# Optimization experiments

Measured on AMD Instinct MI355X. Metric: run time of the kernel, lower is better.

The kernel has to match this reference:

```python
import jax, jax.numpy as jnp
from jax import lax
import numpy as np

WS = (4, 4, 4)          # window size (wd, wh, ww)
DIM = 192               # input channels
HEADS = 6
EPS = 1e-5


def _rel_pos_index(ws):
    coords = np.stack(np.meshgrid(np.arange(ws[0]), np.arange(ws[1]), np.arange(ws[2]), indexing='ij'))
    flat = coords.reshape(3, -1)                              # (3, N)
    rel = (flat[:, :, None] - flat[:, None, :]).transpose(1, 2, 0).astype(np.int64)  # (N, N, 3)
    rel[..., 0] += ws[0] - 1
    rel[..., 1] += ws[1] - 1
    rel[..., 2] += ws[2] - 1
    rel[..., 0] *= (2 * ws[1] - 1) * (2 * ws[2] - 1)
    rel[..., 1] *= (2 * ws[2] - 1)
    return jnp.asarray(rel.sum(-1))                           # (N, N)

REL_IDX = _rel_pos_index(WS)


def _ln(x, g, b):
    m = x.mean(-1, keepdims=True)
    v = x.var(-1, keepdims=True)
    return (x - m) * lax.rsqrt(v + EPS) * g + b


def _inorm(x):  # InstanceNorm3d, affine=False: normalize over spatial dims per (b, c)
    m = x.mean(axis=(2, 3, 4), keepdims=True)
    v = x.var(axis=(2, 3, 4), keepdims=True)
    return (x - m) * lax.rsqrt(v + EPS)


def _gelu(x):
    return jax.nn.gelu(x, approximate=False)


def _win_to_vol(xw, b, d, h, w):
    # (b*d*h*w, wd*wh*ww, c) -> (b, c, d*wd, h*wh, w*ww)
    wd, wh, ww = WS
    c = xw.shape[-1]
    x = xw.reshape(b, d, h, w, wd, wh, ww, c)
    x = x.transpose(0, 7, 1, 4, 2, 5, 3, 6)
    return x.reshape(b, c, d * wd, h * wh, w * ww)


def _vol_to_win(vol):
    # (b, c, D, H, W) -> (b*d*h*w, wd*wh*ww, c)
    wd, wh, ww = WS
    b, c, Dv, Hv, Wv = vol.shape
    x = vol.reshape(b, c, Dv // wd, wd, Hv // wh, wh, Wv // ww, ww)
    x = x.transpose(0, 2, 4, 6, 3, 5, 7, 1)
    return x.reshape(-1, wd * wh * ww, c)


def _conv1x1(x, w, b):  # x: (b,c,D,H,W), w: (c_in, c_out)
    return jnp.einsum('bcdhw,co->bodhw', x, w) + b[None, :, None, None, None]


def _forward(x, w_pattn, b_pattn, g_aln, b_aln, w_pcnn, b_pcnn, g_cln, b_cln,
             dw_w, dw_b, ci_w1, ci_b1, ci_w2, ci_b2, pj_w, pj_b, qkv_w, qkv_b,
             si_w1, si_b1, si_w2, si_b2, g_anorm, b_anorm, w_proj, b_proj, rpb,
             D, H, W):
    wd, wh, ww = WS
    d, h, w = D // wd, H // wh, W // ww
    Bwin, N, _ = x.shape
    b = Bwin // (d * h * w)

    x_atten = _ln(x @ w_pattn + b_pattn, g_aln, b_aln)          # (Bwin, N, 96)
    x_cnn = _ln(x @ w_pcnn + b_pcnn, g_cln, b_cln)              # (Bwin, N, 192)

    vol = _win_to_vol(x_cnn, b, d, h, w)                        # (b, 192, D, H, W)
    vol = lax.conv_general_dilated(vol, dw_w, (1, 1, 1), [(1, 1)] * 3,
                                   feature_group_count=DIM,
                                   dimension_numbers=('NCDHW', 'OIDHW', 'NCDHW'))
    vol = vol + dw_b[None, :, None, None, None]
    vol = _gelu(_inorm(vol))

    pooled = vol.mean(axis=(2, 3, 4))                           # (b, 192)
    ci = _gelu(pooled @ ci_w1 + ci_b1) @ ci_w2 + ci_b2          # (b, 96)
    x_cnn = _conv1x1(vol, pj_w, pj_b)                           # (b, 96, D, H, W)

    C = x_atten.shape[-1]
    hd = C // HEADS
    qkv = (x_atten @ qkv_w + qkv_b).reshape(Bwin, N, 3, HEADS, hd).transpose(2, 0, 3, 1, 4)
    q, k, v = qkv[0], qkv[1], qkv[2]                            # (Bwin, heads, N, hd)

    gate = jax.nn.sigmoid(ci).reshape(b, 1, HEADS, 1, hd)
    v = (v.reshape(b, -1, HEADS, N, hd) * gate).reshape(Bwin, HEADS, N, hd)

    attn = jnp.einsum('bhnd,bhmd->bhnm', q * (hd ** -0.5), k)
    bias = rpb[REL_IDX.reshape(-1)].reshape(N, N, HEADS).transpose(2, 0, 1)
    attn = jax.nn.softmax(attn + bias[None], axis=-1)
    x_atten = jnp.einsum('bhnm,bhmd->bnhd', attn, v).reshape(Bwin, N, C)

    sp = _win_to_vol(x_atten, b, d, h, w)                       # (b, 96, D, H, W)
    si = _conv1x1(sp, si_w1, si_b1)
    si = _gelu(_inorm(si))
    si = _conv1x1(si, si_w2, si_b2)                             # (b, 1, D, H, W)
    x_cnn = _inorm(jax.nn.sigmoid(si) * x_cnn)
    x_cnn = _vol_to_win(x_cnn)                                  # (Bwin, N, 96)

    x_atten = _ln(x_atten, g_anorm, b_anorm)
    return jnp.concatenate([x_atten, x_cnn], axis=-1) @ w_proj + b_proj


def setup_inputs() -> dict:
    key = jax.random.key(0)
    ks = jax.random.split(key, 16)
    def p(i, shape, s=0.02):
        return jax.random.normal(ks[i], shape, jnp.float32) * s
    return {
        'x': jax.random.normal(ks[0], (2048, 64, 192), jnp.float32),
        'w_pattn': p(1, (192, 96)), 'b_pattn': jnp.zeros((96,), jnp.float32),
        'g_aln': jnp.ones((96,), jnp.float32), 'b_aln': jnp.zeros((96,), jnp.float32),
        'w_pcnn': p(2, (192, 192)), 'b_pcnn': jnp.zeros((192,), jnp.float32),
        'g_cln': jnp.ones((192,), jnp.float32), 'b_cln': jnp.zeros((192,), jnp.float32),
        'dw_w': p(3, (192, 1, 3, 3, 3)), 'dw_b': jnp.zeros((192,), jnp.float32),
        'ci_w1': p(4, (192, 24)), 'ci_b1': jnp.zeros((24,), jnp.float32),
        'ci_w2': p(5, (24, 96)), 'ci_b2': jnp.zeros((96,), jnp.float32),
        'pj_w': p(6, (192, 96)), 'pj_b': jnp.zeros((96,), jnp.float32),
        'qkv_w': p(7, (96, 288)), 'qkv_b': jnp.zeros((288,), jnp.float32),
        'si_w1': p(8, (96, 12)), 'si_b1': jnp.zeros((12,), jnp.float32),
        'si_w2': p(9, (12, 1)), 'si_b2': jnp.zeros((1,), jnp.float32),
        'g_anorm': jnp.ones((96,), jnp.float32), 'b_anorm': jnp.zeros((96,), jnp.float32),
        'w_proj': p(10, (192, 192)), 'b_proj': jnp.zeros((192,), jnp.float32),
        'rpb': p(11, (343, 6)),
        'D': 32, 'H': 32, 'W': 32,
    }


def reference(x, w_pattn, b_pattn, g_aln, b_aln, w_pcnn, b_pcnn, g_cln, b_cln,
              dw_w, dw_b, ci_w1, ci_b1, ci_w2, ci_b2, pj_w, pj_b, qkv_w, qkv_b,
              si_w1, si_b1, si_w2, si_b2, g_anorm, b_anorm, w_proj, b_proj, rpb,
              D, H, W):
    return _forward(x, w_pattn, b_pattn, g_aln, b_aln, w_pcnn, b_pcnn, g_cln, b_cln,
                    dw_w, dw_b, ci_w1, ci_b1, ci_w2, ci_b2, pj_w, pj_b, qkv_w, qkv_b,
                    si_w1, si_b1, si_w2, si_b2, g_anorm, b_anorm, w_proj, b_proj, rpb,
                    D, H, W)
```

## Files before the change

kernel.cpp:

```cpp
#include <hip/hip_runtime.h>
#include <hip/hip_bf16.h>
#include <math.h>

#define EPS 1e-5f
#define XAS 97
#define QS 17
#define SS 65

typedef __attribute__((ext_vector_type(8))) short short8;
typedef __attribute__((ext_vector_type(4))) float f32x4;

__device__ __forceinline__ float gelu_f(float x){
    return 0.5f*x*(1.0f+erff(x*0.7071067811865475f));
}
__device__ __forceinline__ float sigmoid_f(float x){
    return 1.0f/(1.0f+__expf(-x));
}
__device__ __forceinline__ int row_to_bv(int r){
    int wi = r >> 6, n = r & 63;
    int b = wi >> 9, rem = wi & 511;
    int zd = rem >> 6, yh = (rem >> 3) & 7, xw = rem & 7;
    int wz = n >> 4, wy = (n >> 2) & 3, wx = n & 3;
    int Dz = (zd<<2)+wz, Hy = (yh<<2)+wy, Wx = (xw<<2)+wx;
    return (b<<15) + (Dz<<10) + (Hy<<5) + Wx;
}
__device__ __forceinline__ int relidx(int i,int j){
    int zi=i>>4, yi=(i>>2)&3, xi=i&3;
    int zj=j>>4, yj=(j>>2)&3, xj=j&3;
    return ((zi-zj+3)*7+(yi-yj+3))*7+(xi-xj+3);
}
__device__ __forceinline__ void split8(const float* p, short8& hi, short8& lo){
    union{short8 v; __hip_bfloat16 b[8];} uh, ul;
    #pragma unroll
    for(int i=0;i<8;i++){
        float v=p[i];
        __hip_bfloat16 h=__float2bfloat16(v);
        uh.b[i]=h;
        ul.b[i]=__float2bfloat16(v-__bfloat162float(h));
    }
    hi=uh.v; lo=ul.v;
}

__global__ __launch_bounds__(256) void kprep1(const float* __restrict__ w1,
    const float* __restrict__ w2, __hip_bfloat16* __restrict__ WThi,
    __hip_bfloat16* __restrict__ WTlo)
{
    int i=blockIdx.x*256+threadIdx.x;
    int n=i/192, k=i-n*192;
    float v=(n<96)? w1[k*96+n] : w2[k*192+(n-96)];
    __hip_bfloat16 hb=__float2bfloat16(v);
    WThi[i]=hb;
    WTlo[i]=__float2bfloat16(v-__bfloat162float(hb));
}

__global__ __launch_bounds__(256) void kprepq(const float* __restrict__ w,
    __hip_bfloat16* __restrict__ WThi, __hip_bfloat16* __restrict__ WTlo)
{
    int i=blockIdx.x*256+threadIdx.x;
    int n=i/96, k=i-n*96;
    float v=w[k*288+n];
    __hip_bfloat16 hb=__float2bfloat16(v);
    WThi[i]=hb;
    WTlo[i]=__float2bfloat16(v-__bfloat162float(hb));
}

__global__ __launch_bounds__(256) void kprepp(const float* __restrict__ w,
    __hip_bfloat16* __restrict__ WThi, __hip_bfloat16* __restrict__ WTlo)
{
    int i=blockIdx.x*256+threadIdx.x;
    int n=i/192, k=i-n*192;
    float v=w[k*96+n];
    __hip_bfloat16 hb=__float2bfloat16(v);
    WThi[i]=hb;
    WTlo[i]=__float2bfloat16(v-__bfloat162float(hb));
}


__global__ __launch_bounds__(256,4) void k1_mfma(const float* __restrict__ x,
    const __hip_bfloat16* __restrict__ WThi, const __hip_bfloat16* __restrict__ WTlo,
    const float* __restrict__ b1, const float* __restrict__ g1, const float* __restrict__ bb1,
    const float* __restrict__ b2, const float* __restrict__ g2, const float* __restrict__ bb2,
    float* __restrict__ xa, float* __restrict__ vol)
{
    __shared__ short bs[288*64];
    int tid=threadIdx.x;
    int row0=blockIdx.x*64;
    int wave=tid>>6, lane=tid&63, quad=lane>>4, l16=lane&15;
    const short* Whi=(const short*)WThi;
    const short* Wlo=(const short*)WTlo;
    f32x4 acc[18];
    #pragma unroll
    for(int j=0;j<18;j++) acc[j]=(f32x4){0.f,0.f,0.f,0.f};
    const float* aptr = x + (size_t)(row0+wave*16+l16)*192 + quad*8;
    int rbase = l16*64 + ((quad ^ (l16&7))<<3);
    for(int t=0;t<6;t++){
        float av[8];
        *(f32x4*)&av[0]=*(const f32x4*)(aptr + t*32);
        *(f32x4*)&av[4]=*(const f32x4*)(aptr + t*32 + 4);
        if(t) __syncthreads();
        #pragma unroll
        for(int it=0;it<9;it++){
            int u=tid+it*256;
            int n=u>>3, gi=u&7;
            const short* src=(gi<4?Whi:Wlo) + n*192 + t*32 + (gi&3)*8;
            *(short8*)&bs[n*64 + ((gi^(n&7))<<3)] = *(const short8*)src;
        }
        __syncthreads();
        short8 ahi, alo;
        split8(av, ahi, alo);
        #pragma unroll
        for(int j=0;j<18;j++){
            int idx=j*1024+rbase;
            short8 bhi = *(const short8*)&bs[idx];
            short8 blo = *(const short8*)&bs[idx^32];
            acc[j]=__builtin_amdgcn_mfma_f32_16x16x32_bf16(ahi,bhi,acc[j],0,0,0);
            acc[j]=__builtin_amdgcn_mfma_f32_16x16x32_bf16(ahi,blo,acc[j],0,0,0);
            acc[j]=__builtin_amdgcn_mfma_f32_16x16x32_bf16(alo,bhi,acc[j],0,0,0);
        }
    }
    float bias[18];
    #pragma unroll
    for(int j=0;j<18;j++){ int c=j*16+l16; bias[j]=(c<96)? b1[c] : b2[c-96]; }
    #pragma unroll
    for(int reg=0; reg<4; reg++){
        int grow=row0 + wave*16 + quad*4 + reg;
        float va[6];
        float s=0.f, ss=0.f;
        #pragma unroll
        for(int j=0;j<6;j++){ float v=acc[j][reg]+bias[j]; va[j]=v; s+=v; ss+=v*v; }
        #pragma unroll
        for(int o=1;o<16;o<<=1){ s+=__shfl_xor(s,o); ss+=__shfl_xor(ss,o); }
        float m=s*(1.f/96.f), var=ss*(1.f/96.f)-m*m, rstd=rsqrtf(var+EPS);
        #pragma unroll
        for(int j=0;j<6;j++){
            int c=j*16+l16;
            xa[(size_t)grow*96+c]=(va[j]-m)*rstd*g1[c]+bb1[c];
        }
        float vc[12];
        s=0.f; ss=0.f;
        #pragma unroll
        for(int j=0;j<12;j++){ float v=acc[6+j][reg]+bias[6+j]; vc[j]=v; s+=v; ss+=v*v; }
        #pragma unroll
        for(int o=1;o<16;o<<=1){ s+=__shfl_xor(s,o); ss+=__shfl_xor(ss,o); }
        float m2=s*(1.f/192.f), var2=ss*(1.f/192.f)-m2*m2, rstd2=rsqrtf(var2+EPS);
        int bv=row_to_bv(grow);
        #pragma unroll
        for(int j=0;j<12;j++){
            int c=j*16+l16;
            vol[(size_t)bv*192+c]=(vc[j]-m2)*rstd2*g2[c]+bb2[c];
        }
    }
}

__global__ __launch_bounds__(192) void k2_dwconv(const float* __restrict__ vin,
        const float* __restrict__ wd_, const float* __restrict__ bd,
        float* __restrict__ vout)
{
    int c=threadIdx.x;
    int blk=blockIdx.x;
    int Hy=blk&31, Dz=(blk>>5)&31, b=blk>>10;
    float wreg[27];
    #pragma unroll
    for(int t=0;t<27;t++) wreg[t]=wd_[c*27+t];
    float bias=bd[c];
    const float* base=vin + ((size_t)b<<15)*192;
    int voff[9]; bool vld[9];
    #pragma unroll
    for(int i=0;i<9;i++){
        int zz=Dz+i/3-1, yy=Hy+i%3-1;
        vld[i]=(zz>=0&&zz<32&&yy>=0&&yy<32);
        voff[i]=(zz<<10)+(yy<<5);
    }
    float prv[9],cur[9],nxt[9];
    #pragma unroll
    for(int i=0;i<9;i++){
        prv[i]=0.f;
        cur[i]= vld[i]? base[(size_t)(voff[i])*192+c]   : 0.f;
        nxt[i]= vld[i]? base[(size_t)(voff[i]+1)*192+c] : 0.f;
    }
    size_t obase=((size_t)((b<<15)+(Dz<<10)+(Hy<<5)))*192 + c;
    for(int wx=0;wx<32;wx++){
        float o=bias;
        #pragma unroll
        for(int i=0;i<9;i++) o += prv[i]*wreg[i*3] + cur[i]*wreg[i*3+1] + nxt[i]*wreg[i*3+2];
        vout[obase + (size_t)wx*192] = o;
        #pragma unroll
        for(int i=0;i<9;i++){ prv[i]=cur[i]; cur[i]=nxt[i]; }
        int wn=wx+2;
        #pragma unroll
        for(int i=0;i<9;i++) nxt[i]=(vld[i]&&wn<32)? base[(size_t)(voff[i]+wn)*192+c] : 0.f;
    }
}

__global__ __launch_bounds__(192) void k3_stats(const float* __restrict__ v,
      float* __restrict__ sum, float* __restrict__ sumsq)
{
    int c=threadIdx.x;
    int chunk=blockIdx.x, b=blockIdx.y;
    float s=0.f,ss=0.f;
    const float* p = v + (((size_t)b<<15) + (size_t)chunk*256)*192 + c;
    for(int i=0;i<256;i++){ float t=p[(size_t)i*192]; s+=t; ss+=t*t; }
    atomicAdd(&sum[b*192+c], s);
    atomicAdd(&sumsq[b*192+c], ss);
}

__global__ void k_finalize(const float* __restrict__ sum, const float* __restrict__ sumsq,
                           float* __restrict__ mean, float* __restrict__ rstd, int n, float inv)
{
    int i = blockIdx.x*blockDim.x + threadIdx.x;
    if(i<n){ float m=sum[i]*inv; float v=sumsq[i]*inv - m*m; mean[i]=m; rstd[i]=rsqrtf(v+EPS); }
}

__global__ __launch_bounds__(192) void k4_apply(float* __restrict__ v,
      const float* __restrict__ mean, const float* __restrict__ rstd, float* __restrict__ pooled)
{
    int c=threadIdx.x; int chunk=blockIdx.x, b=blockIdx.y;
    float m=mean[b*192+c], r=rstd[b*192+c];
    float s=0.f;
    float* p = v + (((size_t)b<<15)+(size_t)chunk*256)*192 + c;
    for(int i=0;i<256;i++){
        float t=(p[(size_t)i*192]-m)*r;
        t=gelu_f(t);
        p[(size_t)i*192]=t; s+=t;
    }
    atomicAdd(&pooled[b*192+c], s);
}

__global__ __launch_bounds__(128) void k4b_gate(const float* __restrict__ pooled,
   const float* __restrict__ w1,const float* __restrict__ b1,
   const float* __restrict__ w2,const float* __restrict__ b2, float* __restrict__ gate)
{
    __shared__ float pm[192];
    __shared__ float h[24];
    int b=blockIdx.x, t=threadIdx.x;
    for(int i=t;i<192;i+=128) pm[i]=pooled[b*192+i]*(1.f/32768.f);
    __syncthreads();
    if(t<24){ float a=b1[t]; for(int k=0;k<192;k++) a+=pm[k]*w1[k*24+t]; h[t]=gelu_f(a); }
    __syncthreads();
    if(t<96){ float a=b2[t]; for(int j=0;j<24;j++) a+=h[j]*w2[j*96+t]; gate[b*96+t]=sigmoid_f(a); }
}

__global__ __launch_bounds__(256,4) void kqkv(const float* __restrict__ xa,
    const __hip_bfloat16* __restrict__ WThi, const __hip_bfloat16* __restrict__ WTlo,
    const float* __restrict__ bias_, const float* __restrict__ gate,
    __hip_bfloat16* __restrict__ qkv)
{
    __shared__ short bs[288*64];
    int tid=threadIdx.x;
    int row0=blockIdx.x*64;
    int wave=tid>>6, lane=tid&63, quad=lane>>4, l16=lane&15;
    const short* Whi=(const short*)WThi;
    const short* Wlo=(const short*)WTlo;
    f32x4 acc[18];
    #pragma unroll
    for(int j=0;j<18;j++) acc[j]=(f32x4){0.f,0.f,0.f,0.f};
    const float* aptr = xa + (size_t)(row0+wave*16+l16)*96 + quad*8;
    int rbase = l16*64 + ((quad ^ (l16&7))<<3);
    for(int t=0;t<3;t++){
        float av[8];
        *(f32x4*)&av[0]=*(const f32x4*)(aptr + t*32);
        *(f32x4*)&av[4]=*(const f32x4*)(aptr + t*32 + 4);
        if(t) __syncthreads();
        #pragma unroll
        for(int it=0;it<9;it++){
            int u=tid+it*256;
            int n=u>>3, gi=u&7;
            const short* src=(gi<4?Whi:Wlo) + n*96 + t*32 + (gi&3)*8;
            *(short8*)&bs[n*64 + ((gi^(n&7))<<3)] = *(const short8*)src;
        }
        __syncthreads();
        short8 ahi, alo;
        split8(av, ahi, alo);
        #pragma unroll
        for(int j=0;j<18;j++){
            int idx=j*1024+rbase;
            short8 bhi = *(const short8*)&bs[idx];
            short8 blo = *(const short8*)&bs[idx^32];
            acc[j]=__builtin_amdgcn_mfma_f32_16x16x32_bf16(ahi,bhi,acc[j],0,0,0);
            acc[j]=__builtin_amdgcn_mfma_f32_16x16x32_bf16(ahi,blo,acc[j],0,0,0);
            acc[j]=__builtin_amdgcn_mfma_f32_16x16x32_bf16(alo,bhi,acc[j],0,0,0);
        }
    }
    int b = row0>>15;
    float gv[6];
    #pragma unroll
    for(int j=0;j<6;j++) gv[j]=gate[b*96 + j*16 + l16];
    #pragma unroll
    for(int j=0;j<18;j++){
        float bb=bias_[j*16+l16];
        int which=j/6;
        #pragma unroll
        for(int reg=0;reg<4;reg++){
            int row=row0+wave*16+quad*4+reg;
            int wi=row>>6, n=row&63;
            float v=acc[j][reg]+bb;
            if(which==0) v*=0.25f;
            else if(which==2) v*=gv[j-12];
            qkv[((size_t)(wi*18+j)<<10) + (n<<4) + l16]=__float2bfloat16(v);
        }
    }
}

__global__ __launch_bounds__(256) void k6_attn(const __hip_bfloat16* __restrict__ qkv,
    const float* __restrict__ rpb, float* __restrict__ ato)
{
    __shared__ float sq[64*QS], sk[64*QS], sv[64*QS];
    __shared__ float sS[64*SS];
    int tid=threadIdx.x;
    int wi=blockIdx.x;
    for(int h=0;h<6;h++){
        __syncthreads();
        for(int i=tid;i<3*1024;i+=256){
            int which=i>>10, r=i&1023; int n=r>>4, e=r&15;
            float val=__bfloat162float(qkv[((size_t)(wi*18+which*6+h)<<10) + r]);
            if(which==0) sq[n*QS+e]=val; else if(which==1) sk[n*QS+e]=val; else sv[n*QS+e]=val;
        }
        __syncthreads();
        {
            int ti=tid>>4, tj=tid&15;
            int i0=ti*4, j0=tj*4;
            float a[4][4]={};
            #pragma unroll
            for(int e=0;e<16;e++){
                float qv[4], kv[4];
                #pragma unroll
                for(int ii=0;ii<4;ii++) qv[ii]=sq[(i0+ii)*QS+e];
                #pragma unroll
                for(int jj=0;jj<4;jj++) kv[jj]=sk[(j0+jj)*QS+e];
                #pragma unroll
                for(int ii=0;ii<4;ii++)
                    #pragma unroll
                    for(int jj=0;jj<4;jj++) a[ii][jj]+=qv[ii]*kv[jj];
            }
            #pragma unroll
            for(int ii=0;ii<4;ii++)
                #pragma unroll
                for(int jj=0;jj<4;jj++)
                    sS[(i0+ii)*SS+j0+jj]=a[ii][jj]+rpb[relidx(i0+ii,j0+jj)*6+h];
        }
        __syncthreads();
        {
            int i=tid>>2, j0=(tid&3)<<4;
            float mx=-1e30f;
            for(int jj=0;jj<16;jj++) mx=fmaxf(mx,sS[i*SS+j0+jj]);
            for(int o=1;o<4;o<<=1) mx=fmaxf(mx,__shfl_xor(mx,o));
            float sum=0.f;
            for(int jj=0;jj<16;jj++){float p=__expf(sS[i*SS+j0+jj]-mx); sS[i*SS+j0+jj]=p; sum+=p;}
            for(int o=1;o<4;o<<=1) sum+=__shfl_xor(sum,o);
            float inv=1.f/sum;
            for(int jj=0;jj<16;jj++) sS[i*SS+j0+jj]*=inv;
        }
        __syncthreads();
        {
            int i=tid&63, e0=(tid>>6)<<2;
            float o0=0.f,o1=0.f,o2=0.f,o3=0.f;
            for(int j=0;j<64;j++){
                float p=sS[i*SS+j];
                o0+=p*sv[j*QS+e0];o1+=p*sv[j*QS+e0+1];o2+=p*sv[j*QS+e0+2];o3+=p*sv[j*QS+e0+3];
            }
            float* dst=&ato[((size_t)(wi*64+i))*96 + (h<<4) + e0];
            dst[0]=o0;dst[1]=o1;dst[2]=o2;dst[3]=o3;
        }
    }
}

__global__ __launch_bounds__(256) void k5_pj(const float* __restrict__ vin,
    const __hip_bfloat16* __restrict__ WThi, const __hip_bfloat16* __restrict__ WTlo,
    const float* __restrict__ bias_, float* __restrict__ out)
{
    __shared__ short bs[96*64];
    int tid=threadIdx.x;
    int row0=blockIdx.x*64;
    int wave=tid>>6, lane=tid&63, quad=lane>>4, l16=lane&15;
    const short* Whi=(const short*)WThi;
    const short* Wlo=(const short*)WTlo;
    f32x4 acc[6];
    #pragma unroll
    for(int j=0;j<6;j++) acc[j]=(f32x4){0.f,0.f,0.f,0.f};
    const float* aptr = vin + (size_t)(row0+wave*16+l16)*192 + quad*8;
    int rbase = l16*64 + ((quad ^ (l16&7))<<3);
    for(int t=0;t<6;t++){
        float av[8];
        *(f32x4*)&av[0]=*(const f32x4*)(aptr + t*32);
        *(f32x4*)&av[4]=*(const f32x4*)(aptr + t*32 + 4);
        if(t) __syncthreads();
        #pragma unroll
        for(int it=0;it<3;it++){
            int u=tid+it*256;
            int n=u>>3, gi=u&7;
            const short* src=(gi<4?Whi:Wlo) + n*192 + t*32 + (gi&3)*8;
            *(short8*)&bs[n*64 + ((gi^(n&7))<<3)] = *(const short8*)src;
        }
        __syncthreads();
        short8 ahi, alo;
        split8(av, ahi, alo);
        #pragma unroll
        for(int j=0;j<6;j++){
            int idx=j*1024+rbase;
            short8 bhi = *(const short8*)&bs[idx];
            short8 blo = *(const short8*)&bs[idx^32];
            acc[j]=__builtin_amdgcn_mfma_f32_16x16x32_bf16(ahi,bhi,acc[j],0,0,0);
            acc[j]=__builtin_amdgcn_mfma_f32_16x16x32_bf16(ahi,blo,acc[j],0,0,0);
            acc[j]=__builtin_amdgcn_mfma_f32_16x16x32_bf16(alo,bhi,acc[j],0,0,0);
        }
    }
    #pragma unroll
    for(int j=0;j<6;j++){
        int cc=j*16+l16;
        float bb=bias_[cc];
        #pragma unroll
        for(int reg=0;reg<4;reg++){
            int row=row0+wave*16+quad*4+reg;
            out[(size_t)row*96+cc]=acc[j][reg]+bb;
        }
    }
}

__global__ __launch_bounds__(192) void k7a_si(const float* __restrict__ ato,
    const float* __restrict__ w1, const float* __restrict__ b1,
    float* __restrict__ si12, float* __restrict__ siSum, float* __restrict__ siSumsq)
{
    __shared__ float sa[64*XAS];
    __shared__ float sw[96*12];
    __shared__ float red[24];
    int tid=threadIdx.x, wi=blockIdx.x, b=wi>>9;
    for(int i=tid;i<64*96;i+=192){ int n=i/96,c=i-n*96; sa[n*XAS+c]=ato[((size_t)(wi*64+n))*96+c]; }
    for(int i=tid;i<96*12;i+=192) sw[i]=w1[i];
    if(tid<24) red[tid]=0.f;
    __syncthreads();
    #pragma unroll
    for(int j=0;j<4;j++){
        int o=tid+192*j; int n=o/12, cc=o-n*12;
        float a=b1[cc];
        for(int k=0;k<96;k++) a+=sa[n*XAS+k]*sw[k*12+cc];
        atomicAdd(&red[cc],a);
        atomicAdd(&red[12+cc],a*a);
        int bv=row_to_bv(wi*64+n);
        si12[(size_t)bv*12+cc]=a;
    }
    __syncthreads();
    if(tid<12){ atomicAdd(&siSum[b*12+tid],red[tid]); atomicAdd(&siSumsq[b*12+tid],red[12+tid]); }
}

__global__ __launch_bounds__(256) void k7d_sig(const float* __restrict__ si12,
  const float* __restrict__ mean, const float* __restrict__ rstd,
  const float* __restrict__ w2, const float* __restrict__ b2, float* __restrict__ sig)
{
    int bv=blockIdx.x*256+threadIdx.x;
    int b=bv>>15;
    float a=b2[0];
    #pragma unroll
    for(int c=0;c<12;c++){
        float t=(si12[(size_t)bv*12+c]-mean[b*12+c])*rstd[b*12+c];
        a+=gelu_f(t)*w2[c];
    }
    sig[bv]=sigmoid_f(a);
}

__global__ __launch_bounds__(192) void k8_gstats(const float* __restrict__ pj,
   const float* __restrict__ sig, float* __restrict__ gSum, float* __restrict__ gSumsq)
{
    int tid=threadIdx.x; int c=tid%96, vh=tid/96;
    int chunk=blockIdx.x, b=blockIdx.y;
    float s=0.f,ss=0.f;
    for(int i=0;i<128;i++){
        int v=chunk*256 + i*2 + vh;
        int bv=(b<<15)+v;
        float t=sig[bv]*pj[(size_t)bv*96+c];
        s+=t; ss+=t*t;
    }
    atomicAdd(&gSum[b*96+c],s); atomicAdd(&gSumsq[b*96+c],ss);
}

__global__ __launch_bounds__(256) void kprep(const float* __restrict__ wp,
                                             __hip_bfloat16* __restrict__ WT)
{
    int i=blockIdx.x*256+threadIdx.x;
    int n=i/192, k=i-n*192;
    WT[n*192+k]=__float2bfloat16(wp[k*192+n]);
}

__global__ __launch_bounds__(256) void k9a2_gather(float* atoU,
  const float* __restrict__ pj, const float* __restrict__ sig,
  const float* __restrict__ gMean, const float* __restrict__ gRstd,
  const float* __restrict__ ga, const float* __restrict__ bba)
{
    int tid=threadIdx.x; int row0=blockIdx.x*32;
    int rr=tid>>3, part=tid&7;
    int r=row0+rr;
    __hip_bfloat16* U=(__hip_bfloat16*)atoU;
    float av[12];
    #pragma unroll
    for(int j=0;j<12;j++) av[j]=atoU[(size_t)r*96+part*12+j];
    float s=0.f, ss=0.f;
    #pragma unroll
    for(int j=0;j<12;j++){ s+=av[j]; ss+=av[j]*av[j]; }
    #pragma unroll
    for(int o=1;o<8;o<<=1){ s+=__shfl_xor(s,o); ss+=__shfl_xor(ss,o); }
    float m=s*(1.f/96.f), var=ss*(1.f/96.f)-m*m, rstd=rsqrtf(var+EPS);
    int bv=row_to_bv(r); int b=bv>>15;
    float sg=sig[bv];
    float cv[12];
    #pragma unroll
    for(int j=0;j<12;j++){
        int c=part*12+j;
        float t=sg*pj[(size_t)bv*96+c];
        cv[j]=(t-gMean[b*96+c])*gRstd[b*96+c];
    }
    #pragma unroll
    for(int j=0;j<12;j++){
        int c=part*12+j;
        U[(size_t)r*192+c]=__float2bfloat16((av[j]-m)*rstd*ga[c]+bba[c]);
    }
    #pragma unroll
    for(int j=0;j<12;j++){
        int c=part*12+j;
        U[(size_t)r*192+96+c]=__float2bfloat16(cv[j]);
    }
}

__global__ __launch_bounds__(256) void k9b_mfma(const __hip_bfloat16* __restrict__ Ubf,
   const __hip_bfloat16* __restrict__ WT, const float* __restrict__ bp,
   float* __restrict__ out)
{
    int tid=threadIdx.x;
    int wave=tid>>6, lane=tid&63;
    int quad=lane>>4, l16=lane&15;
    int rowA = blockIdx.x*64 + wave*16 + l16;
    const short* Us=(const short*)Ubf;
    const short* Ws=(const short*)WT;
    f32x4 acc[12];
    #pragma unroll
    for(int j=0;j<12;j++) acc[j]=(f32x4){0.f,0.f,0.f,0.f};
    #pragma unroll
    for(int t=0;t<6;t++){
        int k0=t*32;
        short8 a = *(const short8*)(Us + (size_t)rowA*192 + k0 + quad*8);
        #pragma unroll
        for(int j=0;j<12;j++){
            short8 bfr = *(const short8*)(Ws + (size_t)(j*16+l16)*192 + k0 + quad*8);
            acc[j]=__builtin_amdgcn_mfma_f32_16x16x32_bf16(a,bfr,acc[j],0,0,0);
        }
    }
    int mbase = blockIdx.x*64 + wave*16 + quad*4;
    #pragma unroll
    for(int j=0;j<12;j++){
        int n=j*16+l16;
        float bias=bp[n];
        #pragma unroll
        for(int r2=0;r2<4;r2++){
            out[(size_t)(mbase+r2)*192 + n] = acc[j][r2] + bias;
        }
    }
}

extern "C" void kernel_launch(void* const* d_in, const int* in_sizes, int n_in,
                              void* d_out, int out_size, void* d_ws, size_t ws_size,
                              hipStream_t stream)
{
    const float* x      =(const float*)d_in[0];
    const float* w_pattn=(const float*)d_in[1];
    const float* b_pattn=(const float*)d_in[2];
    const float* g_aln  =(const float*)d_in[3];
    const float* b_aln  =(const float*)d_in[4];
    const float* w_pcnn =(const float*)d_in[5];
    const float* b_pcnn =(const float*)d_in[6];
    const float* g_cln  =(const float*)d_in[7];
    const float* b_cln  =(const float*)d_in[8];
    const float* dw_w   =(const float*)d_in[9];
    const float* dw_b   =(const float*)d_in[10];
    const float* ci_w1  =(const float*)d_in[11];
    const float* ci_b1  =(const float*)d_in[12];
    const float* ci_w2  =(const float*)d_in[13];
    const float* ci_b2  =(const float*)d_in[14];
    const float* pj_w   =(const float*)d_in[15];
    const float* pj_b   =(const float*)d_in[16];
    const float* qkv_w  =(const float*)d_in[17];
    const float* qkv_b  =(const float*)d_in[18];
    const float* si_w1  =(const float*)d_in[19];
    const float* si_b1  =(const float*)d_in[20];
    const float* si_w2  =(const float*)d_in[21];
    const float* si_b2  =(const float*)d_in[22];
    const float* g_anorm=(const float*)d_in[23];
    const float* b_anorm=(const float*)d_in[24];
    const float* w_proj =(const float*)d_in[25];
    const float* b_proj =(const float*)d_in[26];
    const float* rpb    =(const float*)d_in[27];
    (void)in_sizes; (void)n_in; (void)out_size; (void)ws_size;

    float* ws  =(float*)d_ws;
    float* vol =(float*)d_out;
    float* XA   = ws;
    float* VOLA = ws + 12582912;
    __hip_bfloat16* QKV = (__hip_bfloat16*)(ws + 12582912);
    float* PJ   = ws + 12582912;
    float* SI12 = ws + 25165824;
    float* SIG  = ws + 26738688;
    __hip_bfloat16* WT = (__hip_bfloat16*)(ws + 25165824);
    __hip_bfloat16* WTPHI = (__hip_bfloat16*)(ws + 26869760);
    __hip_bfloat16* WTPLO = WTPHI + 18432;
    float* Z0   = ws + 31457280;
    float* IN_SUM   = Z0;        float* IN_SUMSQ = Z0+768;
    float* POOLED   = Z0+1536;
    float* SI_SUM   = Z0+2304;   float* SI_SUMSQ = Z0+2352;
    float* G_SUM    = Z0+2400;   float* G_SUMSQ  = Z0+2784;
    float* NZ   = ws + 31460448;
    float* IN_MEAN  = NZ;        float* IN_RSTD  = NZ+768;
    float* GATE     = NZ+1536;
    float* SI_MEAN  = NZ+1920;   float* SI_RSTD  = NZ+1968;
    float* G_MEAN   = NZ+2016;   float* G_RSTD   = NZ+2400;
    __hip_bfloat16* WTQHI = (__hip_bfloat16*)(ws + 31463248);
    __hip_bfloat16* WTQLO = WTQHI + 27648;

    __hip_bfloat16* WT1hi=(__hip_bfloat16*)d_out;
    __hip_bfloat16* WT1lo=WT1hi+55296;
    kprep1<<<216,256,0,stream>>>(w_pattn,w_pcnn,WT1hi,WT1lo);
    k1_mfma<<<2048,256,0,stream>>>(x,WT1hi,WT1lo,b_pattn,g_aln,b_aln,
                                   b_pcnn,g_cln,b_cln,XA,VOLA);
    k2_dwconv<<<4096,192,0,stream>>>(VOLA,dw_w,dw_b,vol);
    hipMemsetAsync((void*)Z0, 0, 3168*sizeof(float), stream);
    kprepq<<<108,256,0,stream>>>(qkv_w,WTQHI,WTQLO);
    k3_stats<<<dim3(128,4),192,0,stream>>>(vol,IN_SUM,IN_SUMSQ);
    k_finalize<<<3,256,0,stream>>>(IN_SUM,IN_SUMSQ,IN_MEAN,IN_RSTD,768,1.f/32768.f);
    k4_apply<<<dim3(128,4),192,0,stream>>>(vol,IN_MEAN,IN_RSTD,POOLED);
    k4b_gate<<<4,128,0,stream>>>(POOLED,ci_w1,ci_b1,ci_w2,ci_b2,GATE);
    kqkv<<<2048,256,0,stream>>>(XA,WTQHI,WTQLO,qkv_b,GATE,QKV);
    k6_attn<<<2048,256,0,stream>>>(QKV,rpb,XA);
    kprepp<<<72,256,0,stream>>>(pj_w,WTPHI,WTPLO);
    k5_pj<<<2048,256,0,stream>>>(vol,WTPHI,WTPLO,pj_b,PJ);
    k7a_si<<<2048,192,0,stream>>>(XA,si_w1,si_b1,SI12,SI_SUM,SI_SUMSQ);
    k_finalize<<<1,64,0,stream>>>(SI_SUM,SI_SUMSQ,SI_MEAN,SI_RSTD,48,1.f/32768.f);
    k7d_sig<<<512,256,0,stream>>>(SI12,SI_MEAN,SI_RSTD,si_w2,si_b2,SIG);
    kprep<<<144,256,0,stream>>>(w_proj,WT);
    k8_gstats<<<dim3(128,4),192,0,stream>>>(PJ,SIG,G_SUM,G_SUMSQ);
    k_finalize<<<2,256,0,stream>>>(G_SUM,G_SUMSQ,G_MEAN,G_RSTD,384,1.f/32768.f);
    k9a2_gather<<<4096,256,0,stream>>>(XA,PJ,SIG,G_MEAN,G_RSTD,g_anorm,b_anorm);
    k9b_mfma<<<2048,256,0,stream>>>((const __hip_bfloat16*)XA,WT,b_proj,vol);
}
```

Measured before the change: 995.0 us.

## Use bf16 MFMA for window attention with register softmax

Rewrites the per-window attention kernel so QK^T and PV use 16x16x32 bf16 MFMA instructions instead of scalar FP32 FMAs from shared memory. Softmax now runs in registers with cross-lane shuffles, and probabilities are written as bf16 into an XOR-swizzled LDS tile, with V stored transposed. This removes two block barriers per head and most of the LDS traffic. In exchange, the probabilities are rounded to bf16, which lowers accuracy, and half the lanes feed zero padding into the QK MFMA because the head dimension is only 16.

After: 843.6 us. -15.2%, faster.

```diff
diff --git a/kernel.cpp b/kernel.cpp
--- a/kernel.cpp
+++ b/kernel.cpp
@@ -4,8 +4,6 @@
 
 #define EPS 1e-5f
 #define XAS 97
-#define QS 17
-#define SS 65
 
 typedef __attribute__((ext_vector_type(8))) short short8;
 typedef __attribute__((ext_vector_type(4))) float f32x4;
@@ -15,6 +13,10 @@
 }
 __device__ __forceinline__ float sigmoid_f(float x){
     return 1.0f/(1.0f+__expf(-x));
+}
+__device__ __forceinline__ short bf16s(float x){
+    __hip_bfloat16 h=__float2bfloat16(x);
+    return *(short*)&h;
 }
 __device__ __forceinline__ int row_to_bv(int r){
     int wi = r >> 6, n = r & 63;
@@ -304,63 +306,73 @@
 __global__ __launch_bounds__(256) void k6_attn(const __hip_bfloat16* __restrict__ qkv,
     const float* __restrict__ rpb, float* __restrict__ ato)
 {
-    __shared__ float sq[64*QS], sk[64*QS], sv[64*QS];
-    __shared__ float sS[64*SS];
+    __shared__ short qs[1024];
+    __shared__ short ks_[1024];
+    __shared__ short vt[1024];
+    __shared__ short ps[4096];
     int tid=threadIdx.x;
     int wi=blockIdx.x;
+    int wave=tid>>6, lane=tid&63, quad=lane>>4, l16=lane&15;
+    int ridx[4][4];
+    #pragma unroll
+    for(int jt=0;jt<4;jt++)
+        #pragma unroll
+        for(int reg=0;reg<4;reg++)
+            ridx[jt][reg]=relidx(wave*16+quad*4+reg, jt*16+l16);
+    const short* qkvs=(const short*)qkv + ((size_t)(wi*18)<<10);
+    int vn=tid>>2, ve0=(tid&3)<<2;
     for(int h=0;h<6;h++){
         __syncthreads();
-        for(int i=tid;i<3*1024;i+=256){
-            int which=i>>10, r=i&1023; int n=r>>4, e=r&15;
-            float val=__bfloat162float(qkv[((size_t)(wi*18+which*6+h)<<10) + r]);
-            if(which==0) sq[n*QS+e]=val; else if(which==1) sk[n*QS+e]=val; else sv[n*QS+e]=val;
+        {
+            const short* src = qkvs + (((tid<128?0:6)+h)<<10) + ((tid&127)<<3);
+            short8 v8=*(const short8*)src;
+            *(short8*)((tid<128? qs: ks_) + ((tid&127)<<3)) = v8;
+            const short* vsrc = qkvs + ((12+h)<<10) + (vn<<4) + ve0;
+            #pragma unroll
+            for(int j=0;j<4;j++){
+                int e=ve0+j;
+                vt[(e*64+vn) ^ ((e&7)<<3)] = vsrc[j];
+            }
         }
         __syncthreads();
-        {
-            int ti=tid>>4, tj=tid&15;
-            int i0=ti*4, j0=tj*4;
-            float a[4][4]={};
+        short8 zf=(short8){0,0,0,0,0,0,0,0};
+        short8 afr = (quad<2)? *(const short8*)&qs[(wave*16+l16)*16 + quad*8] : zf;
+        f32x4 accs[4];
+        #pragma unroll
+        for(int jt=0;jt<4;jt++){
+            short8 bfr = (quad<2)? *(const short8*)&ks_[(jt*16+l16)*16 + quad*8] : zf;
+            accs[jt]=__builtin_amdgcn_mfma_f32_16x16x32_bf16(afr,bfr,(f32x4){0.f,0.f,0.f,0.f},0,0,0);
+        }
+        #pragma unroll
+        for(int reg=0;reg<4;reg++){
+            float v0=accs[0][reg]+rpb[ridx[0][reg]*6+h];
+            float v1=accs[1][reg]+rpb[ridx[1][reg]*6+h];
+            float v2=accs[2][reg]+rpb[ridx[2][reg]*6+h];
+            float v3=accs[3][reg]+rpb[ridx[3][reg]*6+h];
+            float mx=fmaxf(fmaxf(v0,v1),fmaxf(v2,v3));
             #pragma unroll
-            for(int e=0;e<16;e++){
-                float qv[4], kv[4];
-                #pragma unroll
-                for(int ii=0;ii<4;ii++) qv[ii]=sq[(i0+ii)*QS+e];
-                #pragma unroll
-                for(int jj=0;jj<4;jj++) kv[jj]=sk[(j0+jj)*QS+e];
-                #pragma unroll
-                for(int ii=0;ii<4;ii++)
-                    #pragma unroll
-                    for(int jj=0;jj<4;jj++) a[ii][jj]+=qv[ii]*kv[jj];
-            }
+            for(int o=1;o<16;o<<=1) mx=fmaxf(mx,__shfl_xor(mx,o));
+            float e0=__expf(v0-mx),e1=__expf(v1-mx),e2=__expf(v2-mx),e3=__expf(v3-mx);
+            float sm=e0+e1+e2+e3;
             #pragma unroll
-            for(int ii=0;ii<4;ii++)
-                #pragma unroll
-                for(int jj=0;jj<4;jj++)
-                    sS[(i0+ii)*SS+j0+jj]=a[ii][jj]+rpb[relidx(i0+ii,j0+jj)*6+h];
-        }
-        __syncthreads();
-        {
-            int i=tid>>2, j0=(tid&3)<<4;
-            float mx=-1e30f;
-            for(int jj=0;jj<16;jj++) mx=fmaxf(mx,sS[i*SS+j0+jj]);
-            for(int o=1;o<4;o<<=1) mx=fmaxf(mx,__shfl_xor(mx,o));
-            float sum=0.f;
-            for(int jj=0;jj<16;jj++){float p=__expf(sS[i*SS+j0+jj]-mx); sS[i*SS+j0+jj]=p; sum+=p;}
-            for(int o=1;o<4;o<<=1) sum+=__shfl_xor(sum,o);
-            float inv=1.f/sum;
-            for(int jj=0;jj<16;jj++) sS[i*SS+j0+jj]*=inv;
-        }
-        __syncthreads();
-        {
-            int i=tid&63, e0=(tid>>6)<<2;
-            float o0=0.f,o1=0.f,o2=0.f,o3=0.f;
-            for(int j=0;j<64;j++){
-                float p=sS[i*SS+j];
-                o0+=p*sv[j*QS+e0];o1+=p*sv[j*QS+e0+1];o2+=p*sv[j*QS+e0+2];o3+=p*sv[j*QS+e0+3];
-            }
-            float* dst=&ato[((size_t)(wi*64+i))*96 + (h<<4) + e0];
-            dst[0]=o0;dst[1]=o1;dst[2]=o2;dst[3]=o3;
-        }
+            for(int o=1;o<16;o<<=1) sm+=__shfl_xor(sm,o);
+            float inv=1.f/sm;
+            int i=wave*16+quad*4+reg, ib=(i&7)<<3;
+            ps[(i*64 +      l16) ^ ib]=bf16s(e0*inv);
+            ps[(i*64 + 16 + l16) ^ ib]=bf16s(e1*inv);
+            ps[(i*64 + 32 + l16) ^ ib]=bf16s(e2*inv);
+            ps[(i*64 + 48 + l16) ^ ib]=bf16s(e3*inv);
+        }
+        asm volatile("s_waitcnt lgkmcnt(0)" ::: "memory");
+        __builtin_amdgcn_sched_barrier(0);
+        f32x4 acco=(f32x4){0.f,0.f,0.f,0.f};
+        #pragma unroll
+        for(int ks2=0;ks2<2;ks2++){
+            short8 a=*(const short8*)&vt[(l16*64 + ks2*32 + quad*8) ^ ((l16&7)<<3)];
+            short8 b=*(const short8*)&ps[((wave*16+l16)*64 + ks2*32 + quad*8) ^ ((l16&7)<<3)];
+            acco=__builtin_amdgcn_mfma_f32_16x16x32_bf16(a,b,acco,0,0,0);
+        }
+        *(f32x4*)&ato[((size_t)(wi*64 + wave*16 + l16))*96 + (h<<4) + quad*4] = acco;
     }
 }
 
```
